# Optimization experiments

Measured on AMD Instinct MI355X. Metric: run time of the kernel, lower is better.

Reference implementation:

```python
import jax, jax.numpy as jnp
import numpy as np

EPS = 1e-5  # torch LayerNorm default

def _layernorm(x, g, b):
    mu = jnp.mean(x, axis=-1, keepdims=True)
    var = jnp.mean(jnp.square(x - mu), axis=-1, keepdims=True)
    return (x - mu) * jax.lax.rsqrt(var + EPS) * g + b

def _gelu(x):
    return jax.nn.gelu(x, approximate=False)  # torch nn.GELU default is exact erf

def setup_inputs() -> dict:
    B, S, D, F = 2, 128, 64, 256
    key = jax.random.key(0)
    ks = jax.random.split(key, 8)
    def xavier(k, fan_in, fan_out, gain=1.0):
        lim = gain * np.sqrt(6.0 / (fan_in + fan_out))
        return jax.random.uniform(k, (fan_in, fan_out), jnp.float32, -lim, lim)
    return {
        "q": jax.random.normal(ks[0], (B, S, D), jnp.float32),
        # gauge generator MLP: Linear(2D, F) -> GELU -> Linear(F, D*D)
        "gw1": xavier(ks[1], 2 * D, F),
        "gb1": jnp.zeros((F,), jnp.float32),
        "gw2": xavier(ks[2], F, D * D, gain=0.01),  # nn.init.xavier_uniform_(gain=0.01)
        "gb2": jnp.zeros((D * D,), jnp.float32),    # nn.init.zeros_
        # block MLP: Linear(D, F) -> GELU -> Linear(F, D)
        "mw1": xavier(ks[3], D, F),
        "mb1": jnp.zeros((F,), jnp.float32),
        "mw2": xavier(ks[4], F, D),
        "mb2": jnp.zeros((D,), jnp.float32),
        # LayerNorms
        "ln1_g": jnp.ones((D,), jnp.float32),
        "ln1_b": jnp.zeros((D,), jnp.float32),
        "ln2_g": jnp.ones((D,), jnp.float32),
        "ln2_b": jnp.zeros((D,), jnp.float32),
    }

def reference(q, gw1, gb1, gw2, gb2, mw1, mb1, mw2, mb2, ln1_g, ln1_b, ln2_g, ln2_b):
    B, S, D = q.shape
    phi = q
    # pairwise features: cat(phi_i, phi_j) -> (B, S, S, 2D)
    phi_i = jnp.broadcast_to(phi[:, :, None, :], (B, S, S, D))
    phi_j = jnp.broadcast_to(phi[:, None, :, :], (B, S, S, D))
    pairs = jnp.concatenate([phi_i, phi_j], axis=-1)
    # gauge MLP -> U_ij in (B, S, S, D, D)
    h = _gelu(pairs @ gw1 + gb1)
    U = (h @ gw2 + gb2).reshape(B, S, S, D, D)
    # aggregate: sum_j U_ij @ phi_j  (contract d with phi feature dim)
    agg = jnp.einsum('bijde,bjd->bie', U, phi)
    # dropout in eval mode = identity
    phi = _layernorm(phi + agg, ln1_g, ln1_b)
    mlp_out = _gelu(phi @ mw1 + mb1) @ mw2 + mb2
    return _layernorm(phi + mlp_out, ln2_g, ln2_b)
```

## Files before the change

kernel.cpp:

```cpp
#include <hip/hip_runtime.h>
#include <hip/hip_bf16.h>
#include <math.h>

namespace {

constexpr int NB = 2, NS = 128, ND = 64, NF = 256;

typedef __attribute__((ext_vector_type(8))) short short8;
typedef __attribute__((ext_vector_type(8))) unsigned short ushort8;
typedef __attribute__((ext_vector_type(4))) float floatx4;

constexpr size_t OFF_W2H  = 0;
constexpr size_t SZ_W2H   = (size_t)NB * NS * NF * ND / 2;
constexpr size_t OFF_P    = OFF_W2H + SZ_W2H;
constexpr size_t SZ_P     = (size_t)NB * NS * NS * ND / 2;
constexpr size_t OFF_AT   = OFF_P + SZ_P;
constexpr size_t SZ_AT    = (size_t)NB * NF * NS;
constexpr size_t OFF_BT   = OFF_AT + SZ_AT;
constexpr size_t SZ_BT    = (size_t)NB * NS * NF;
constexpr size_t OFF_BIAS = OFF_BT + SZ_BT;

__device__ __forceinline__ float gelu_fast(float x) {
  const float xs = fabsf(x) * 0.70710678118654752f;
  const float t = __builtin_amdgcn_rcpf(fmaf(0.3275911f, xs, 1.0f));
  float p = fmaf(1.061405429f, t, -1.453152027f);
  p = fmaf(p, t, 1.421413741f);
  p = fmaf(p, t, -0.284496736f);
  p = fmaf(p, t, 0.254829592f);
  p *= t;
  const float e = __expf(-xs * xs);
  const float erf_ax = fmaf(-p, e, 1.0f);
  const float erf_x = copysignf(erf_ax, x);
  return 0.5f * x * (1.0f + erf_x);
}

__device__ __forceinline__ ushort8 pack_bf16x8(const float v[8]) {
  union { __hip_bfloat162 b2[4]; ushort8 u; } u;
  #pragma unroll
  for (int p = 0; p < 4; ++p)
    u.b2[p] = __float22bfloat162_rn(make_float2(v[2 * p], v[2 * p + 1]));
  return u.u;
}

__device__ __forceinline__ float bf16u_to_f(unsigned short u) {
  return __uint_as_float((unsigned)u << 16);
}

__global__ __launch_bounds__(512) void kA_pre(const float* __restrict__ q,
                                              const float* __restrict__ gw1,
                                              const float* __restrict__ gb1,
                                              const float* __restrict__ gw2,
                                              const float* __restrict__ gb2,
                                              float* __restrict__ A_t,
                                              float* __restrict__ Bt,
                                              unsigned short* __restrict__ W2h,
                                              float* __restrict__ bias_agg) {
  __shared__ __align__(16) unsigned short smem_u[128 * 64 + 8 * 64 * 40];
  float* smf = (float*)smem_u;
  const int t = threadIdx.x, bid = blockIdx.x;

  if (bid < 128) {
    const int b = bid >> 6, ip = bid & 63;
    const int half = t >> 8, f = t & 255;
    const int i = ip * 2 + half;
    float* qrow = smf;
    if (f < 64) qrow[half * 64 + f] = q[((size_t)b * NS + i) * ND + f];
    __syncthreads();
    float a = 0.f, bb = gb1[f];
    #pragma unroll 8
    for (int d = 0; d < ND; ++d) {
      const float qd = qrow[half * 64 + d];
      a  += qd * gw1[d * NF + f];
      bb += qd * gw1[(ND + d) * NF + f];
    }
    A_t[((size_t)b * NF + f) * NS + i] = a;
    Bt[((size_t)b * NS + i) * NF + f] = bb;
  } else if (bid < 192) {
    const int idx = bid - 128;
    const int b = idx >> 5, f0 = (idx & 31) * 8;
    unsigned short* qbf = smem_u;
    unsigned short* Gt  = smem_u + 128 * 64;
    {
      const int jq = t >> 1, half = t & 1;
      const float* src = q + ((size_t)b * NS + jq) * ND + half * 32;
      #pragma unroll
      for (int p = 0; p < 4; ++p) {
        float v[8];
        #pragma unroll
        for (int r = 0; r < 8; ++r) v[r] = src[p * 8 + r];
        const int oct = half * 4 + p;
        const int col = oct ^ (jq & 7);
        *(ushort8*)&qbf[jq * 64 + col * 8] = pack_bf16x8(v);
      }
    }
    const int lane = t & 63, w = t >> 6;
    const int f = f0 + w;
    const int m = lane & 15, quad = lane >> 4;
    const int te = t & 63, tf = t >> 6;
    floatx4 acc[8][4];
    #pragma unroll
    for (int ti = 0; ti < 8; ++ti)
      #pragma unroll
      for (int tn = 0; tn < 4; ++tn) acc[ti][tn] = (floatx4)0.f;

    for (int dc = 0; dc < 2; ++dc) {
      __syncthreads();
      const float* gsrc = gw2 + (size_t)(f0 + tf) * (ND * ND) + (size_t)(dc * 32) * ND + te;
      #pragma unroll
      for (int p = 0; p < 4; ++p) {
        float gv[8];
        #pragma unroll
        for (int r = 0; r < 8; ++r) gv[r] = gsrc[(size_t)(p * 8 + r) * ND];
        *(ushort8*)&Gt[tf * 2560 + te * 40 + p * 8] = pack_bf16x8(gv);
      }
      __syncthreads();
      short8 bfr[4];
      #pragma unroll
      for (int tn = 0; tn < 4; ++tn)
        bfr[tn] = *(const short8*)&Gt[w * 2560 + (tn * 16 + m) * 40 + quad * 8];
      #pragma unroll
      for (int ti = 0; ti < 8; ++ti) {
        const int jr = ti * 16 + m;
        const int col = (dc * 4 + quad) ^ (jr & 7);
        const short8 afr = *(const short8*)&qbf[jr * 64 + col * 8];
        #pragma unroll
        for (int tn = 0; tn < 4; ++tn)
          acc[ti][tn] = __builtin_amdgcn_mfma_f32_16x16x32_bf16(afr, bfr[tn],
                                                                acc[ti][tn], 0, 0, 0);
      }
    }
    __hip_bfloat16* Wh = (__hip_bfloat16*)W2h;
    #pragma unroll
    for (int ti = 0; ti < 8; ++ti)
      #pragma unroll
      for (int r = 0; r < 4; ++r) {
        const int jr = ti * 16 + quad * 4 + r;
        __hip_bfloat16* dst = Wh + ((size_t)(b * NS + jr) * NF + f) * ND;
        #pragma unroll
        for (int tn = 0; tn < 4; ++tn)
          dst[tn * 16 + m] = __float2bfloat16(acc[ti][tn][r]);
      }
  } else {
    const int b = bid - 192;
    float* qs = smf;
    float* colsum = smf + NS * ND;
    for (int r = 0; r < 16; ++r) qs[t + r * 512] = q[(size_t)b * NS * ND + t + r * 512];
    __syncthreads();
    if (t < ND) {
      float s = 0.f;
      for (int jj = 0; jj < NS; ++jj) s += qs[jj * ND + t];
      colsum[t] = s;
    }
    __syncthreads();
    if (t < ND) {
      float a2 = 0.f;
      for (int d = 0; d < ND; ++d) a2 += gb2[d * ND + t] * colsum[d];
      bias_agg[b * ND + t] = a2;
    }
  }
}

constexpr int HLD = 72;

__global__ __launch_bounds__(512) void k2_main(const float* __restrict__ A_t,
                                               const float* __restrict__ Bt,
                                               const unsigned short* __restrict__ W2h,
                                               unsigned short* __restrict__ P) {
  const int b = blockIdx.x / NS, j = blockIdx.x % NS;
  const int t = threadIdx.x;
  const int lane = t & 63, w = t >> 6;
  __shared__ float Btj[NF];
  __shared__ __align__(16) unsigned short Hc[NS * HLD];
  __shared__ __align__(16) unsigned short Wc[ND * HLD];
  if (t < NF) Btj[t] = Bt[((size_t)b * NS + j) * NF + t];

  const unsigned short* Whbj = W2h + (size_t)(b * NS + j) * NF * ND;
  const float* Ab = A_t + (size_t)b * NF * NS;

  const int wi = (w & 3) * 32, we = (w >> 2) * 32;
  const int m = lane & 15, quad = lane >> 4;
  const int hi = (w & 1) * 64 + lane, hoct0 = w >> 1;
  const int wei = t & 63, woct = w;

  floatx4 acc[2][2];
  #pragma unroll
  for (int a0 = 0; a0 < 2; ++a0)
    #pragma unroll
    for (int a1 = 0; a1 < 2; ++a1) acc[a0][a1] = (floatx4)0.f;

  unsigned short wvv[8];
  #pragma unroll
  for (int r = 0; r < 8; ++r)
    wvv[r] = Whbj[(size_t)(woct * 8 + r) * ND + wei];
  float ar[2][8];
  #pragma unroll
  for (int s = 0; s < 2; ++s)
    #pragma unroll
    for (int r = 0; r < 8; ++r)
      ar[s][r] = Ab[(size_t)((hoct0 + 4 * s) * 8 + r) * NS + hi];
  __syncthreads();

  for (int c = 0; c < NF / 64; ++c) {
    ushort8 hv[2];
    #pragma unroll
    for (int s = 0; s < 2; ++s) {
      float hvf[8];
      #pragma unroll
      for (int r = 0; r < 8; ++r) {
        const int fl = c * 64 + (hoct0 + 4 * s) * 8 + r;
        hvf[r] = gelu_fast(ar[s][r] + Btj[fl]);
      }
      hv[s] = pack_bf16x8(hvf);
    }
    union { unsigned short a[8]; ushort8 v; } wu;
    #pragma unroll
    for (int r = 0; r < 8; ++r) wu.a[r] = wvv[r];
    if (c > 0) __syncthreads();
    *(ushort8*)&Wc[wei * HLD + woct * 8] = wu.v;
    *(ushort8*)&Hc[hi * HLD + hoct0 * 8] = hv[0];
    *(ushort8*)&Hc[hi * HLD + (hoct0 + 4) * 8] = hv[1];
    if (c < NF / 64 - 1) {
      #pragma unroll
      for (int r = 0; r < 8; ++r)
        wvv[r] = Whbj[(size_t)((c + 1) * 64 + woct * 8 + r) * ND + wei];
      #pragma unroll
      for (int s = 0; s < 2; ++s)
        #pragma unroll
        for (int r = 0; r < 8; ++r)
          ar[s][r] = Ab[(size_t)((c + 1) * 64 + (hoct0 + 4 * s) * 8 + r) * NS + hi];
    }
    __syncthreads();
    #pragma unroll
    for (int kk = 0; kk < 2; ++kk) {
      short8 afr[2], bfr[2];
      #pragma unroll
      for (int ti = 0; ti < 2; ++ti)
        afr[ti] = *(const short8*)&Hc[(wi + ti * 16 + m) * HLD + kk * 32 + quad * 8];
      #pragma unroll
      for (int te = 0; te < 2; ++te)
        bfr[te] = *(const short8*)&Wc[(we + te * 16 + m) * HLD + kk * 32 + quad * 8];
      #pragma unroll
      for (int ti = 0; ti < 2; ++ti)
        #pragma unroll
        for (int te = 0; te < 2; ++te)
          acc[ti][te] = __builtin_amdgcn_mfma_f32_16x16x32_bf16(
              afr[ti], bfr[te], acc[ti][te], 0, 0, 0);
    }
  }
  __hip_bfloat16* Pbj = (__hip_bfloat16*)(P + (size_t)(b * NS + j) * NS * ND);
  #pragma unroll
  for (int ti = 0; ti < 2; ++ti)
    #pragma unroll
    for (int te = 0; te < 2; ++te)
      #pragma unroll
      for (int r = 0; r < 4; ++r) {
        const int row = wi + ti * 16 + quad * 4 + r;
        const int col = we + te * 16 + m;
        Pbj[(size_t)row * ND + col] = __float2bfloat16(acc[ti][te][r]);
      }
}

__global__ __launch_bounds__(512) void k3_epi(const float* __restrict__ q,
                                              const unsigned short* __restrict__ P,
                                              const float* __restrict__ bias_agg,
                                              const float* __restrict__ mw1,
                                              const float* __restrict__ mb1,
                                              const float* __restrict__ mw2,
                                              const float* __restrict__ mb2,
                                              const float* __restrict__ ln1g,
                                              const float* __restrict__ ln1b,
                                              const float* __restrict__ ln2g,
                                              const float* __restrict__ ln2b,
                                              float* __restrict__ out) {
  const int b = blockIdx.x / NS, i = blockIdx.x % NS;
  const int t = threadIdx.x;
  const int e = t & 63, g = t >> 6;
  __shared__ float red[8 * ND];
  __shared__ float phi1[ND];
  __shared__ float hid[NF];
  const unsigned short* Pb = P + (size_t)b * NS * NS * ND;
  float s = 0.f;
  #pragma unroll 4
  for (int m0 = 0; m0 < 16; ++m0) {
    const int jj = g * 16 + m0;
    s += bf16u_to_f(Pb[((size_t)jj * NS + i) * ND + e]);
  }
  red[t] = s;
  __syncthreads();
  if (t < ND) {
    float agg = bias_agg[b * ND + e];
    #pragma unroll
    for (int gg = 0; gg < 8; ++gg) agg += red[gg * ND + e];
    const float x = q[((size_t)b * NS + i) * ND + e] + agg;
    float sum = x, sumsq = x * x;
    #pragma unroll
    for (int off = 32; off >= 1; off >>= 1) {
      sum += __shfl_xor(sum, off);
      sumsq += __shfl_xor(sumsq, off);
    }
    const float mu = sum * (1.f / 64.f);
    const float var = sumsq * (1.f / 64.f) - mu * mu;
    const float inv = rsqrtf(var + 1e-5f);
    phi1[e] = (x - mu) * inv * ln1g[e] + ln1b[e];
  }
  __syncthreads();
  if (t < NF) {
    float h = mb1[t];
    #pragma unroll 8
    for (int d = 0; d < ND; ++d) h += phi1[d] * mw1[d * NF + t];
    hid[t] = gelu_fast(h);
  }
  __syncthreads();
  {
    float p = 0.f;
    #pragma unroll 8
    for (int m0 = 0; m0 < 32; ++m0) {
      const int f = g * 32 + m0;
      p += hid[f] * mw2[f * ND + e];
    }
    red[t] = p;
  }
  __syncthreads();
  if (t < ND) {
    float mlp = mb2[e];
    #pragma unroll
    for (int gg = 0; gg < 8; ++gg) mlp += red[gg * ND + e];
    const float x = phi1[e] + mlp;
    float sum = x, sumsq = x * x;
    #pragma unroll
    for (int off = 32; off >= 1; off >>= 1) {
      sum += __shfl_xor(sum, off);
      sumsq += __shfl_xor(sumsq, off);
    }
    const float mu = sum * (1.f / 64.f);
    const float var = sumsq * (1.f / 64.f) - mu * mu;
    const float inv = rsqrtf(var + 1e-5f);
    out[((size_t)b * NS + i) * ND + e] = (x - mu) * inv * ln2g[e] + ln2b[e];
  }
}

}

extern "C" void kernel_launch(void* const* d_in, const int* in_sizes, int n_in,
                              void* d_out, int out_size, void* d_ws, size_t ws_size,
                              hipStream_t stream) {
  const float* q    = (const float*)d_in[0];
  const float* gw1  = (const float*)d_in[1];
  const float* gb1  = (const float*)d_in[2];
  const float* gw2  = (const float*)d_in[3];
  const float* gb2  = (const float*)d_in[4];
  const float* mw1  = (const float*)d_in[5];
  const float* mb1  = (const float*)d_in[6];
  const float* mw2  = (const float*)d_in[7];
  const float* mb2  = (const float*)d_in[8];
  const float* ln1g = (const float*)d_in[9];
  const float* ln1b = (const float*)d_in[10];
  const float* ln2g = (const float*)d_in[11];
  const float* ln2b = (const float*)d_in[12];
  float* out = (float*)d_out;
  float* ws  = (float*)d_ws;

  unsigned short* W2h = (unsigned short*)(ws + OFF_W2H);
  unsigned short* Pp  = (unsigned short*)(ws + OFF_P);
  float* A_t  = ws + OFF_AT;
  float* Bt   = ws + OFF_BT;
  float* bias = ws + OFF_BIAS;

  kA_pre<<<194, 512, 0, stream>>>(q, gw1, gb1, gw2, gb2, A_t, Bt, W2h, bias);
  k2_main<<<NB * NS, 512, 0, stream>>>(A_t, Bt, W2h, Pp);
  k3_epi<<<NB * NS, 512, 0, stream>>>(q, Pp, bias, mw1, mb1, mw2, mb2,
                                      ln1g, ln1b, ln2g, ln2b, out);
}
```

Before: 107.4 us.

## Fuse three kernels into one cooperative kernel with grid-wide syncs

Replaces the three separate launches (precompute, main MFMA contraction, epilogue) with a single cooperative kernel of 256 blocks that uses grid syncs between phases, sharing one static shared-memory buffer. The aim is to remove the launch gaps and tail effects between small kernels. The epilogue's P reduction is also changed to use vectorized 8-wide bf16 loads with a two-level shared-memory reduction. In exchange it adds the cost of grid-wide barriers and fixes the grid at 256 blocks, which must all be co-resident.

```diff
diff --git a/kernel.cpp b/kernel.cpp
--- a/kernel.cpp
+++ b/kernel.cpp
@@ -1,6 +1,9 @@
 #include <hip/hip_runtime.h>
+#include <hip/hip_cooperative_groups.h>
 #include <hip/hip_bf16.h>
 #include <math.h>
+
+namespace cg = cooperative_groups;
 
 namespace {
 
@@ -46,30 +49,36 @@
   return __uint_as_float((unsigned)u << 16);
 }
 
-__global__ __launch_bounds__(512) void kA_pre(const float* __restrict__ q,
-                                              const float* __restrict__ gw1,
-                                              const float* __restrict__ gb1,
-                                              const float* __restrict__ gw2,
-                                              const float* __restrict__ gb2,
-                                              float* __restrict__ A_t,
-                                              float* __restrict__ Bt,
-                                              unsigned short* __restrict__ W2h,
-                                              float* __restrict__ bias_agg) {
-  __shared__ __align__(16) unsigned short smem_u[128 * 64 + 8 * 64 * 40];
-  float* smf = (float*)smem_u;
-  const int t = threadIdx.x, bid = blockIdx.x;
+constexpr int HLD = 72;
+
+__global__ __launch_bounds__(512) void k_fused(
+    const float* __restrict__ q,    const float* __restrict__ gw1,
+    const float* __restrict__ gb1,  const float* __restrict__ gw2,
+    const float* __restrict__ gb2,  const float* __restrict__ mw1,
+    const float* __restrict__ mb1,  const float* __restrict__ mw2,
+    const float* __restrict__ mb2,  const float* __restrict__ ln1g,
+    const float* __restrict__ ln1b, const float* __restrict__ ln2g,
+    const float* __restrict__ ln2b, float* __restrict__ out,
+    float* __restrict__ A_t,        float* __restrict__ Bt,
+    unsigned short* __restrict__ W2h, float* __restrict__ bias_agg,
+    unsigned short* __restrict__ P) {
+  __shared__ __align__(16) unsigned char smem_raw[57344];
+  unsigned short* const smem_u = (unsigned short*)smem_raw;
+  float* const smf = (float*)smem_raw;
+  const int t = threadIdx.x;
+  const int bid = blockIdx.x;
 
   if (bid < 128) {
     const int b = bid >> 6, ip = bid & 63;
     const int half = t >> 8, f = t & 255;
     const int i = ip * 2 + half;
     float* qrow = smf;
-    if (f < 64) qrow[half * 64 + f] = q[((size_t)b * NS + i) * ND + f];
+    if (f < ND) qrow[half * ND + f] = q[((size_t)b * NS + i) * ND + f];
     __syncthreads();
     float a = 0.f, bb = gb1[f];
     #pragma unroll 8
     for (int d = 0; d < ND; ++d) {
-      const float qd = qrow[half * 64 + d];
+      const float qd = qrow[half * ND + d];
       a  += qd * gw1[d * NF + f];
       bb += qd * gw1[(ND + d) * NF + f];
     }
@@ -140,7 +149,7 @@
         for (int tn = 0; tn < 4; ++tn)
           dst[tn * 16 + m] = __float2bfloat16(acc[ti][tn][r]);
       }
-  } else {
+  } else if (bid < 194) {
     const int b = bid - 192;
     float* qs = smf;
     float* colsum = smf + NS * ND;
@@ -158,184 +167,187 @@
       bias_agg[b * ND + t] = a2;
     }
   }
-}
-
-constexpr int HLD = 72;
-
-__global__ __launch_bounds__(512) void k2_main(const float* __restrict__ A_t,
-                                               const float* __restrict__ Bt,
-                                               const unsigned short* __restrict__ W2h,
-                                               unsigned short* __restrict__ P) {
-  const int b = blockIdx.x / NS, j = blockIdx.x % NS;
-  const int t = threadIdx.x;
-  const int lane = t & 63, w = t >> 6;
-  __shared__ float Btj[NF];
-  __shared__ __align__(16) unsigned short Hc[NS * HLD];
-  __shared__ __align__(16) unsigned short Wc[ND * HLD];
-  if (t < NF) Btj[t] = Bt[((size_t)b * NS + j) * NF + t];
-
-  const unsigned short* Whbj = W2h + (size_t)(b * NS + j) * NF * ND;
-  const float* Ab = A_t + (size_t)b * NF * NS;
-
-  const int wi = (w & 3) * 32, we = (w >> 2) * 32;
-  const int m = lane & 15, quad = lane >> 4;
-  const int hi = (w & 1) * 64 + lane, hoct0 = w >> 1;
-  const int wei = t & 63, woct = w;
-
-  floatx4 acc[2][2];
-  #pragma unroll
-  for (int a0 = 0; a0 < 2; ++a0)
-    #pragma unroll
-    for (int a1 = 0; a1 < 2; ++a1) acc[a0][a1] = (floatx4)0.f;
-
-  unsigned short wvv[8];
-  #pragma unroll
-  for (int r = 0; r < 8; ++r)
-    wvv[r] = Whbj[(size_t)(woct * 8 + r) * ND + wei];
-  float ar[2][8];
-  #pragma unroll
-  for (int s = 0; s < 2; ++s)
+  __threadfence();
+  cg::this_grid().sync();
+
+  {
+    const int b = bid >> 7, j = bid & (NS - 1);
+    const int lane = t & 63, w = t >> 6;
+    float* const Btj = smf;
+    unsigned short* const Hc = (unsigned short*)(smem_raw + 1024);
+    unsigned short* const Wc = (unsigned short*)(smem_raw + 1024 + NS * HLD * 2);
+    if (t < NF) Btj[t] = Bt[((size_t)b * NS + j) * NF + t];
+
+    const unsigned short* Whbj = W2h + (size_t)(b * NS + j) * NF * ND;
+    const float* Ab = A_t + (size_t)b * NF * NS;
+
+    const int wi = (w & 3) * 32, we = (w >> 2) * 32;
+    const int m = lane & 15, quad = lane >> 4;
+    const int hi = (w & 1) * 64 + lane, hoct0 = w >> 1;
+    const int wei = t & 63, woct = w;
+
+    floatx4 acc[2][2];
+    #pragma unroll
+    for (int a0 = 0; a0 < 2; ++a0)
+      #pragma unroll
+      for (int a1 = 0; a1 < 2; ++a1) acc[a0][a1] = (floatx4)0.f;
+
+    unsigned short wvv[8];
     #pragma unroll
     for (int r = 0; r < 8; ++r)
-      ar[s][r] = Ab[(size_t)((hoct0 + 4 * s) * 8 + r) * NS + hi];
-  __syncthreads();
-
-  for (int c = 0; c < NF / 64; ++c) {
-    ushort8 hv[2];
-    #pragma unroll
-    for (int s = 0; s < 2; ++s) {
-      float hvf[8];
-      #pragma unroll
-      for (int r = 0; r < 8; ++r) {
-        const int fl = c * 64 + (hoct0 + 4 * s) * 8 + r;
-        hvf[r] = gelu_fast(ar[s][r] + Btj[fl]);
-      }
-      hv[s] = pack_bf16x8(hvf);
-    }
-    union { unsigned short a[8]; ushort8 v; } wu;
-    #pragma unroll
-    for (int r = 0; r < 8; ++r) wu.a[r] = wvv[r];
-    if (c > 0) __syncthreads();
-    *(ushort8*)&Wc[wei * HLD + woct * 8] = wu.v;
-    *(ushort8*)&Hc[hi * HLD + hoct0 * 8] = hv[0];
-    *(ushort8*)&Hc[hi * HLD + (hoct0 + 4) * 8] = hv[1];
-    if (c < NF / 64 - 1) {
+      wvv[r] = Whbj[(size_t)(woct * 8 + r) * ND + wei];
+    float ar[2][8];
+    #pragma unroll
+    for (int s = 0; s < 2; ++s)
       #pragma unroll
       for (int r = 0; r < 8; ++r)
-        wvv[r] = Whbj[(size_t)((c + 1) * 64 + woct * 8 + r) * ND + wei];
-      #pragma unroll
-      for (int s = 0; s < 2; ++s)
+        ar[s][r] = Ab[(size_t)((hoct0 + 4 * s) * 8 + r) * NS + hi];
+    __syncthreads();
+
+    for (int c = 0; c < NF / 64; ++c) {
+      ushort8 hv[2];
+      #pragma unroll
+      for (int s = 0; s < 2; ++s) {
+        float hvf[8];
+        #pragma unroll
+        for (int r = 0; r < 8; ++r) {
+          const int fl = c * 64 + (hoct0 + 4 * s) * 8 + r;
+          hvf[r] = gelu_fast(ar[s][r] + Btj[fl]);
+        }
+        hv[s] = pack_bf16x8(hvf);
+      }
+      union { unsigned short a[8]; ushort8 v; } wu;
+      #pragma unroll
+      for (int r = 0; r < 8; ++r) wu.a[r] = wvv[r];
+      if (c > 0) __syncthreads();
+      *(ushort8*)&Wc[wei * HLD + woct * 8] = wu.v;
+      *(ushort8*)&Hc[hi * HLD + hoct0 * 8] = hv[0];
+      *(ushort8*)&Hc[hi * HLD + (hoct0 + 4) * 8] = hv[1];
+      if (c < NF / 64 - 1) {
         #pragma unroll
         for (int r = 0; r < 8; ++r)
-          ar[s][r] = Ab[(size_t)((c + 1) * 64 + (hoct0 + 4 * s) * 8 + r) * NS + hi];
-    }
-    __syncthreads();
-    #pragma unroll
-    for (int kk = 0; kk < 2; ++kk) {
-      short8 afr[2], bfr[2];
-      #pragma unroll
-      for (int ti = 0; ti < 2; ++ti)
-        afr[ti] = *(const short8*)&Hc[(wi + ti * 16 + m) * HLD + kk * 32 + quad * 8];
+          wvv[r] = Whbj[(size_t)((c + 1) * 64 + woct * 8 + r) * ND + wei];
+        #pragma unroll
+        for (int s = 0; s < 2; ++s)
+          #pragma unroll
+          for (int r = 0; r < 8; ++r)
+            ar[s][r] = Ab[(size_t)((c + 1) * 64 + (hoct0 + 4 * s) * 8 + r) * NS + hi];
+      }
+      __syncthreads();
+      #pragma unroll
+      for (int kk = 0; kk < 2; ++kk) {
+        short8 afr[2], bfr[2];
+        #pragma unroll
+        for (int ti = 0; ti < 2; ++ti)
+          afr[ti] = *(const short8*)&Hc[(wi + ti * 16 + m) * HLD + kk * 32 + quad * 8];
+        #pragma unroll
+        for (int te = 0; te < 2; ++te)
+          bfr[te] = *(const short8*)&Wc[(we + te * 16 + m) * HLD + kk * 32 + quad * 8];
+        #pragma unroll
+        for (int ti = 0; ti < 2; ++ti)
+          #pragma unroll
+          for (int te = 0; te < 2; ++te)
+            acc[ti][te] = __builtin_amdgcn_mfma_f32_16x16x32_bf16(
+                afr[ti], bfr[te], acc[ti][te], 0, 0, 0);
+      }
+    }
+    __hip_bfloat16* Pbj = (__hip_bfloat16*)(P + (size_t)(b * NS + j) * NS * ND);
+    #pragma unroll
+    for (int ti = 0; ti < 2; ++ti)
       #pragma unroll
       for (int te = 0; te < 2; ++te)
-        bfr[te] = *(const short8*)&Wc[(we + te * 16 + m) * HLD + kk * 32 + quad * 8];
-      #pragma unroll
-      for (int ti = 0; ti < 2; ++ti)
-        #pragma unroll
-        for (int te = 0; te < 2; ++te)
-          acc[ti][te] = __builtin_amdgcn_mfma_f32_16x16x32_bf16(
-              afr[ti], bfr[te], acc[ti][te], 0, 0, 0);
-    }
+        #pragma unroll
+        for (int r = 0; r < 4; ++r) {
+          const int row = wi + ti * 16 + quad * 4 + r;
+          const int col = we + te * 16 + m;
+          Pbj[(size_t)row * ND + col] = __float2bfloat16(acc[ti][te][r]);
+        }
   }
-  __hip_bfloat16* Pbj = (__hip_bfloat16*)(P + (size_t)(b * NS + j) * NS * ND);
-  #pragma unroll
-  for (int ti = 0; ti < 2; ++ti)
-    #pragma unroll
-    for (int te = 0; te < 2; ++te)
-      #pragma unroll
-      for (int r = 0; r < 4; ++r) {
-        const int row = wi + ti * 16 + quad * 4 + r;
-        const int col = we + te * 16 + m;
-        Pbj[(size_t)row * ND + col] = __float2bfloat16(acc[ti][te][r]);
-      }
-}
-
-__global__ __launch_bounds__(512) void k3_epi(const float* __restrict__ q,
-                                              const unsigned short* __restrict__ P,
-                                              const float* __restrict__ bias_agg,
-                                              const float* __restrict__ mw1,
-                                              const float* __restrict__ mb1,
-                                              const float* __restrict__ mw2,
-                                              const float* __restrict__ mb2,
-                                              const float* __restrict__ ln1g,
-                                              const float* __restrict__ ln1b,
-                                              const float* __restrict__ ln2g,
-                                              const float* __restrict__ ln2b,
-                                              float* __restrict__ out) {
-  const int b = blockIdx.x / NS, i = blockIdx.x % NS;
-  const int t = threadIdx.x;
-  const int e = t & 63, g = t >> 6;
-  __shared__ float red[8 * ND];
-  __shared__ float phi1[ND];
-  __shared__ float hid[NF];
-  const unsigned short* Pb = P + (size_t)b * NS * NS * ND;
-  float s = 0.f;
-  #pragma unroll 4
-  for (int m0 = 0; m0 < 16; ++m0) {
-    const int jj = g * 16 + m0;
-    s += bf16u_to_f(Pb[((size_t)jj * NS + i) * ND + e]);
-  }
-  red[t] = s;
-  __syncthreads();
-  if (t < ND) {
-    float agg = bias_agg[b * ND + e];
-    #pragma unroll
-    for (int gg = 0; gg < 8; ++gg) agg += red[gg * ND + e];
-    const float x = q[((size_t)b * NS + i) * ND + e] + agg;
-    float sum = x, sumsq = x * x;
-    #pragma unroll
-    for (int off = 32; off >= 1; off >>= 1) {
-      sum += __shfl_xor(sum, off);
-      sumsq += __shfl_xor(sumsq, off);
-    }
-    const float mu = sum * (1.f / 64.f);
-    const float var = sumsq * (1.f / 64.f) - mu * mu;
-    const float inv = rsqrtf(var + 1e-5f);
-    phi1[e] = (x - mu) * inv * ln1g[e] + ln1b[e];
-  }
-  __syncthreads();
-  if (t < NF) {
-    float h = mb1[t];
-    #pragma unroll 8
-    for (int d = 0; d < ND; ++d) h += phi1[d] * mw1[d * NF + t];
-    hid[t] = gelu_fast(h);
-  }
-  __syncthreads();
+  __threadfence();
+  cg::this_grid().sync();
+
   {
-    float p = 0.f;
-    #pragma unroll 8
-    for (int m0 = 0; m0 < 32; ++m0) {
-      const int f = g * 32 + m0;
-      p += hid[f] * mw2[f * ND + e];
-    }
-    red[t] = p;
-  }
-  __syncthreads();
-  if (t < ND) {
-    float mlp = mb2[e];
-    #pragma unroll
-    for (int gg = 0; gg < 8; ++gg) mlp += red[gg * ND + e];
-    const float x = phi1[e] + mlp;
-    float sum = x, sumsq = x * x;
-    #pragma unroll
-    for (int off = 32; off >= 1; off >>= 1) {
-      sum += __shfl_xor(sum, off);
-      sumsq += __shfl_xor(sumsq, off);
-    }
-    const float mu = sum * (1.f / 64.f);
-    const float var = sumsq * (1.f / 64.f) - mu * mu;
-    const float inv = rsqrtf(var + 1e-5f);
-    out[((size_t)b * NS + i) * ND + e] = (x - mu) * inv * ln2g[e] + ln2b[e];
+    const int b = bid >> 7, i = bid & (NS - 1);
+    const int e = t & 63, g = t >> 6;
+    float* const red  = smf;
+    float* const red2 = smf + 64 * 72;
+    float* const phi1 = red2 + 8 * 64;
+    float* const hid  = phi1 + ND;
+    const unsigned short* Pb = P + (size_t)b * NS * NS * ND;
+    {
+      const int og = t >> 3, e0 = (t & 7) * 8;
+      float s[8];
+      #pragma unroll
+      for (int k = 0; k < 8; ++k) s[k] = 0.f;
+      #pragma unroll
+      for (int hlf = 0; hlf < 2; ++hlf) {
+        const int jj = og + hlf * 64;
+        const ushort8 v = *(const ushort8*)&Pb[((size_t)jj * NS + i) * ND + e0];
+        #pragma unroll
+        for (int k = 0; k < 8; ++k) s[k] += bf16u_to_f(v[k]);
+      }
+      #pragma unroll
+      for (int k = 0; k < 8; ++k) red[og * 72 + e0 + k] = s[k];
+    }
+    __syncthreads();
+    {
+      const int r = t >> 6;
+      float p = 0.f;
+      #pragma unroll
+      for (int m0 = 0; m0 < 8; ++m0) p += red[(r * 8 + m0) * 72 + e];
+      red2[r * 64 + e] = p;
+    }
+    __syncthreads();
+    if (t < ND) {
+      float agg = bias_agg[b * ND + e];
+      #pragma unroll
+      for (int gg = 0; gg < 8; ++gg) agg += red2[gg * 64 + e];
+      const float x = q[((size_t)b * NS + i) * ND + e] + agg;
+      float sum = x, sumsq = x * x;
+      #pragma unroll
+      for (int off = 32; off >= 1; off >>= 1) {
+        sum += __shfl_xor(sum, off);
+        sumsq += __shfl_xor(sumsq, off);
+      }
+      const float mu = sum * (1.f / 64.f);
+      const float var = sumsq * (1.f / 64.f) - mu * mu;
+      const float inv = rsqrtf(var + 1e-5f);
+      phi1[e] = (x - mu) * inv * ln1g[e] + ln1b[e];
+    }
+    __syncthreads();
+    if (t < NF) {
+      float h = mb1[t];
+      #pragma unroll 8
+      for (int d = 0; d < ND; ++d) h += phi1[d] * mw1[d * NF + t];
+      hid[t] = gelu_fast(h);
+    }
+    __syncthreads();
+    {
+      float p = 0.f;
+      #pragma unroll 8
+      for (int m0 = 0; m0 < 32; ++m0) {
+        const int f = g * 32 + m0;
+        p += hid[f] * mw2[f * ND + e];
+      }
+      red2[t] = p;
+    }
+    __syncthreads();
+    if (t < ND) {
+      float mlp = mb2[e];
+      #pragma unroll
+      for (int gg = 0; gg < 8; ++gg) mlp += red2[gg * 64 + e];
+      const float x = phi1[e] + mlp;
+      float sum = x, sumsq = x * x;
+      #pragma unroll
+      for (int off = 32; off >= 1; off >>= 1) {
+        sum += __shfl_xor(sum, off);
+        sumsq += __shfl_xor(sumsq, off);
+      }
+      const float mu = sum * (1.f / 64.f);
+      const float var = sumsq * (1.f / 64.f) - mu * mu;
+      const float inv = rsqrtf(var + 1e-5f);
+      out[((size_t)b * NS + i) * ND + e] = (x - mu) * inv * ln2g[e] + ln2b[e];
+    }
   }
 }
 
@@ -366,8 +378,11 @@
   float* Bt   = ws + OFF_BT;
   float* bias = ws + OFF_BIAS;
 
-  kA_pre<<<194, 512, 0, stream>>>(q, gw1, gb1, gw2, gb2, A_t, Bt, W2h, bias);
-  k2_main<<<NB * NS, 512, 0, stream>>>(A_t, Bt, W2h, Pp);
-  k3_epi<<<NB * NS, 512, 0, stream>>>(q, Pp, bias, mw1, mb1, mw2, mb2,
-                                      ln1g, ln1b, ln2g, ln2b, out);
-}
+  void* args[] = {(void*)&q,    (void*)&gw1,  (void*)&gb1,  (void*)&gw2,
+                  (void*)&gb2,  (void*)&mw1,  (void*)&mb1,  (void*)&mw2,
+                  (void*)&mb2,  (void*)&ln1g, (void*)&ln1b, (void*)&ln2g,
+                  (void*)&ln2b, (void*)&out,  (void*)&A_t,  (void*)&Bt,
+                  (void*)&W2h,  (void*)&bias, (void*)&Pp};
+  hipLaunchCooperativeKernel((const void*)k_fused, dim3(NB * NS), dim3(512),
+                             args, 0, stream);
+}
```

Measured after the change: 309.5 us. +188.1%, slower.
